# Performance work log

Measured on AMD Instinct MI355X. Metric: run time of the kernel, lower is better.

Reference implementation:

```python
import jax, jax.numpy as jnp
import numpy as np

E, H, KVH, D = 2048, 16, 4, 128      # embed_dim, heads, kv heads, head_dim
HG, R, SYM, VAN = 12, 32, 4, 4       # graph heads, rel_rank, sym heads, vanilla heads
BASE = 10000
EPS = 1e-6


def _rms_norm(x, w):
    # RMSNorm over last dim (head_dim)
    return x * jax.lax.rsqrt(jnp.mean(x * x, axis=-1, keepdims=True) + EPS) * w


def _rotate_half(x):
    x1, x2 = jnp.split(x, 2, axis=-1)
    return jnp.concatenate([-x2, x1], axis=-1)


def _rope(q, k):
    # q, k: [B, H, S, D]
    S = q.shape[2]
    inv_freq = 1.0 / (BASE ** (jnp.arange(0, D, 2, dtype=jnp.float32) / D))
    t = jnp.arange(S, dtype=jnp.float32)
    freqs = jnp.outer(t, inv_freq)                       # [S, D/2]
    emb = jnp.concatenate([freqs, freqs], axis=-1)       # [S, D]
    cos = jnp.cos(emb)[None, None].astype(q.dtype)
    sin = jnp.sin(emb)[None, None].astype(q.dtype)
    return q * cos + _rotate_half(q) * sin, k * cos + _rotate_half(k) * sin


def setup_inputs() -> dict:
    key = jax.random.key(0)
    ks = jax.random.split(key, 9)
    B, S = 1, 2048
    std = 0.02
    return {
        'x': jax.random.normal(ks[0], (B, S, E), jnp.float32),
        'Wq': jax.random.normal(ks[1], (E, E), jnp.float32) * std,
        'Wk': jax.random.normal(ks[2], (KVH * D, E), jnp.float32) * std,
        'Wv': jax.random.normal(ks[3], (KVH * D, E), jnp.float32) * std,
        'Wo': jax.random.normal(ks[4], (E, E), jnp.float32) * std,
        'q_norm_w': jnp.ones((D,), jnp.float32),
        'k_norm_w': jnp.ones((D,), jnp.float32),
        'Wrq': jax.random.normal(ks[5], (HG * R, E), jnp.float32) * 0.01,
        'Wrk': jax.random.normal(ks[6], (HG * R, E), jnp.float32) * 0.01,
        'graph_scale': jax.random.normal(ks[7], (HG,), jnp.float32) * 0.1,
    }


def reference(x, Wq, Wk, Wv, Wo, q_norm_w, k_norm_w, Wrq, Wrk, graph_scale):
    B, S, _ = x.shape
    # projections -> [B, heads, S, D]
    q = (x @ Wq.T).reshape(B, S, H, D).transpose(0, 2, 1, 3)
    k = (x @ Wk.T).reshape(B, S, KVH, D).transpose(0, 2, 1, 3)
    v = (x @ Wv.T).reshape(B, S, KVH, D).transpose(0, 2, 1, 3)
    # QK-norm then RoPE
    q = _rms_norm(q, q_norm_w)
    k = _rms_norm(k, k_norm_w)
    q, k = _rope(q, k)
    # GQA: repeat kv heads
    rep = H // KVH
    k = jnp.repeat(k, rep, axis=1)
    v = jnp.repeat(v, rep, axis=1)
    # low-rank graph bias: [B, HG, S, S]
    Rq = (x @ Wrq.T).reshape(B, S, HG, R).transpose(0, 2, 1, 3)
    Rk = (x @ Wrk.T).reshape(B, S, HG, R).transpose(0, 2, 1, 3)
    bias = jnp.einsum('bhsr,bhtr->bhst', Rq, Rk)
    sym = bias[:, :SYM]
    sym = (sym + sym.transpose(0, 1, 3, 2)) * 0.5
    bias = jnp.concatenate([sym, bias[:, SYM:]], axis=1)
    bias = bias * graph_scale[None, :, None, None]
    # vanilla heads (last VAN heads) get zero bias
    bias = jnp.concatenate([bias, jnp.zeros((B, VAN, S, S), bias.dtype)], axis=1)
    # attention with causal mask
    scale = 1.0 / np.sqrt(D).astype(np.float32)
    scores = jnp.einsum('bhsd,bhtd->bhst', q, k) * scale + bias
    causal = jnp.tril(jnp.ones((S, S), bool))
    scores = jnp.where(causal[None, None], scores, jnp.finfo(scores.dtype).min)
    attn = jax.nn.softmax(scores, axis=-1)
    out = jnp.einsum('bhst,bhtd->bhsd', attn, v)
    out = out.transpose(0, 2, 1, 3).reshape(B, S, E)
    return out @ Wo.T
```

## Files before the change

### kernel.cpp

```cpp
#include <hip/hip_runtime.h>
#include <hip/hip_bf16.h>

typedef __attribute__((ext_vector_type(8))) short short8;
typedef __attribute__((ext_vector_type(4))) float f32x4;
typedef __attribute__((ext_vector_type(4))) unsigned int u32x4;

__device__ __forceinline__ f32x4 mfma16(short8 a, short8 b, f32x4 c) {
  return __builtin_amdgcn_mfma_f32_16x16x32_bf16(a, b, c, 0, 0, 0);
}

__device__ __forceinline__ void gload_lds16(const void* g, void* l) {
  __builtin_amdgcn_global_load_lds(
      (const __attribute__((address_space(1))) void*)g,
      (__attribute__((address_space(3))) void*)l, 16, 0, 0);
}

__device__ __forceinline__ unsigned int bfp(float lo, float hi) {
  return (unsigned int)__builtin_bit_cast(unsigned short, __float2bfloat16(lo)) |
         ((unsigned int)__builtin_bit_cast(unsigned short, __float2bfloat16(hi)) << 16);
}

struct __align__(8) bh4 { __hip_bfloat16 a, b, c, d; };
struct CastSeg { const float* src; __hip_bfloat16* dst; int n4; };
struct CastArgs { CastSeg seg[7]; int tot4; };

__global__ __launch_bounds__(256) void cast_all(CastArgs a) {
  int i = blockIdx.x * 256 + threadIdx.x;
  const int stride = gridDim.x * 256;
  for (; i < a.tot4; i += stride) {
    int j = i, s = 0;
    while (j >= a.seg[s].n4) { j -= a.seg[s].n4; ++s; }
    float4 v = ((const float4*)a.seg[s].src)[j];
    bh4 o{__float2bfloat16(v.x), __float2bfloat16(v.y),
          __float2bfloat16(v.z), __float2bfloat16(v.w)};
    ((bh4*)a.seg[s].dst)[j] = o;
  }
}

__global__ __launch_bounds__(256) void gemm_bt(const __hip_bfloat16* __restrict__ A,
                                               const __hip_bfloat16* __restrict__ B,
                                               float* __restrict__ C,
                                               int N, int K) {
  __shared__ __align__(16) __hip_bfloat16 As[64][32];
  __shared__ __align__(16) __hip_bfloat16 Bs[128][32];

  const int tid = threadIdx.x;
  const int lane = tid & 63, wv = tid >> 6;
  const int wn = wv * 32;
  const int l15 = lane & 15, g = lane >> 4;
  const int mb = blockIdx.y * 64, nb = blockIdx.x * 128;

  const int arow = wv * 16 + (lane >> 2);
  const int brow = wv * 32 + (lane >> 2);
  const int scol = (lane & 3) * 8;
  const __hip_bfloat16* Ap = A + (size_t)(mb + arow) * K + scol;
  const __hip_bfloat16* Bp = B + (size_t)(nb + brow) * K + scol;
  __hip_bfloat16* lA  = &As[wv * 16][0];
  __hip_bfloat16* lB0 = &Bs[wv * 32][0];
  __hip_bfloat16* lB1 = &Bs[wv * 32 + 16][0];

  const f32x4 zf = {0.f, 0.f, 0.f, 0.f};
  f32x4 acc[4][2];
#pragma unroll
  for (int m = 0; m < 4; ++m)
#pragma unroll
    for (int n = 0; n < 2; ++n) acc[m][n] = zf;

  for (int k0 = 0; k0 < K; k0 += 32) {
    __syncthreads();
    gload_lds16(Ap + k0, lA);
    gload_lds16(Bp + k0, lB0);
    gload_lds16(Bp + (size_t)16 * K + k0, lB1);
    __syncthreads();
    short8 af[4], bf[2];
#pragma unroll
    for (int m = 0; m < 4; ++m) af[m] = *(const short8*)&As[m * 16 + l15][g * 8];
#pragma unroll
    for (int n = 0; n < 2; ++n) bf[n] = *(const short8*)&Bs[wn + n * 16 + l15][g * 8];
#pragma unroll
    for (int m = 0; m < 4; ++m)
#pragma unroll
      for (int n = 0; n < 2; ++n) acc[m][n] = mfma16(af[m], bf[n], acc[m][n]);
  }

#pragma unroll
  for (int m = 0; m < 4; ++m)
#pragma unroll
    for (int n = 0; n < 2; ++n)
#pragma unroll
      for (int r = 0; r < 4; ++r)
        C[(size_t)(mb + m * 16 + g * 4 + r) * N + (nb + wn + n * 16 + l15)] =
            acc[m][n][r];
}

__global__ __launch_bounds__(256) void postproc(const float* __restrict__ C1,
                                                const float* __restrict__ qw,
                                                const float* __restrict__ kw,
                                                __hip_bfloat16* __restrict__ qn,
                                                __hip_bfloat16* __restrict__ kn,
                                                __hip_bfloat16* __restrict__ rq,
                                                __hip_bfloat16* __restrict__ rk) {
  constexpr int S = 2048;
  const int s = blockIdx.x;
  const int tid = threadIdx.x;
  const int lane = tid & 63;
  const int wv = tid >> 6;
  const float* row = C1 + (size_t)s * 3840;

  const float f = exp2f(-(float)lane * (13.287712379549449f / 64.0f));
  const float ang = (float)s * f;
  float sn, cs;
  sincosf(ang, &sn, &cs);

  for (int hr = wv; hr < 20; hr += 4) {
    const float* base;
    __hip_bfloat16* dst;
    const float* nw;
    float oscale;
    if (hr < 16) {
      base = row + hr * 128;
      dst = qn + ((size_t)hr * S + s) * 128;
      nw = qw;
      oscale = 0.08838834764831845f;
    } else {
      const int h4 = hr - 16;
      base = row + 2048 + h4 * 128;
      dst = kn + ((size_t)h4 * S + s) * 128;
      nw = kw;
      oscale = 1.0f;
    }
    const float x1 = base[lane], x2 = base[lane + 64];
    float ss = x1 * x1 + x2 * x2;
#pragma unroll
    for (int mk = 1; mk < 64; mk <<= 1) ss += __shfl_xor(ss, mk);
    const float rms = rsqrtf(ss * (1.0f / 128.0f) + 1e-6f);
    const float x1n = x1 * rms * nw[lane];
    const float x2n = x2 * rms * nw[lane + 64];
    dst[lane]      = __float2bfloat16((x1n * cs - x2n * sn) * oscale);
    dst[lane + 64] = __float2bfloat16((x2n * cs + x1n * sn) * oscale);
  }
  for (int i = tid; i < 768; i += 256) {
    if (i < 384) {
      rq[((size_t)(i >> 5) * S + s) * 32 + (i & 31)] = __float2bfloat16(row[3072 + i]);
    } else {
      const int j = i - 384;
      rk[((size_t)(j >> 5) * S + s) * 32 + (j & 31)] = __float2bfloat16(row[3072 + i]);
    }
  }
}

__global__ __launch_bounds__(256) void transpose_v(const float* __restrict__ C1,
                                                   __hip_bfloat16* __restrict__ vt) {
  __shared__ float T[32][129];
  const int b = blockIdx.x;
  const int h4 = b >> 6;
  const int s0 = (b & 63) * 32;
  const int tid = threadIdx.x;
  for (int idx = tid; idx < 4096; idx += 256) {
    const int s = idx >> 7, d = idx & 127;
    T[s][d] = C1[(size_t)(s0 + s) * 3840 + 2560 + h4 * 128 + d];
  }
  __syncthreads();
  for (int j = tid; j < 4096; j += 256) {
    const int d = j >> 5, s = j & 31;
    vt[(size_t)(h4 * 128 + d) * 2048 + s0 + s] = __float2bfloat16(T[s][d]);
  }
}

__global__ __launch_bounds__(256) void attn_kernel(
    const __hip_bfloat16* __restrict__ qn, const __hip_bfloat16* __restrict__ kn,
    const __hip_bfloat16* __restrict__ vt, const __hip_bfloat16* __restrict__ rq,
    const __hip_bfloat16* __restrict__ rk, const float* __restrict__ gsc,
    __hip_bfloat16* __restrict__ ao) {
  constexpr int S = 2048;
  constexpr float L2E = 1.4426950408889634f;
  const int bid = blockIdx.x;
  const int j = bid & 15;
  const int h = ((j & 3) << 2) | (j >> 2);
  const int u = bid >> 4;
  const int qb = (u < 16) ? (31 - u) : (u - 16);
  const int tid = threadIdx.x;
  const int lane = tid & 63;
  const int wv = tid >> 6;
  const int qs = qb * 64 + wv * 16;
  const int l15 = lane & 15, g = lane >> 4;
  const int h4 = h >> 2;
  const bool has_bias = (h < 12);
  const bool symh = (h < 4);
  const float gs = has_bias ? gsc[h] : 0.0f;
  const f32x4 zf = {0.f, 0.f, 0.f, 0.f};

  __shared__ __align__(16) char KsRaw[2][16384];
  __shared__ __align__(16) char VsRaw[2][16384];

  const int sxk = ((tid >> 4) & 7) << 4;
  const int sxv = ((tid >> 3) & 7) << 4;
  const int k_wr = (tid * 16) ^ sxk;
  const int v_wr = (tid * 16) ^ sxv;
  const int kx = (l15 & 7) << 4;

  const __hip_bfloat16* kbase = kn + (size_t)h4 * S * 128;
  const __hip_bfloat16* vbase = vt + (size_t)h4 * 128 * S;
  const __hip_bfloat16* rkp   = rk + (size_t)h * S * 32;
  const __hip_bfloat16* rqp   = rq + (size_t)h * S * 32;

  short8 qf[4];
  {
    const __hip_bfloat16* qrow = qn + ((size_t)h * S + qs + l15) * 128 + g * 8;
#pragma unroll
    for (int kc = 0; kc < 4; ++kc) qf[kc] = *(const short8*)(qrow + kc * 32);
  }
  short8 rqA = {}, rkA = {};
  if (has_bias) rqA = *(const short8*)(rqp + (size_t)(qs + l15) * 32 + g * 8);
  if (symh)     rkA = *(const short8*)(rkp + (size_t)(qs + l15) * 32 + g * 8);

  float lp = 0.0f;
  f32x4 acc[8];
#pragma unroll
  for (int fb = 0; fb < 8; ++fb) acc[fb] = zf;

  const int nt = qb + 1;

  short8 kreg[4], vreg[4];
  auto load_kv = [&](int tb) {
#pragma unroll
    for (int c = 0; c < 4; ++c) {
      kreg[c] = *(const short8*)(kbase + ((size_t)(tb + c * 16 + (tid >> 4))) * 128 + (tid & 15) * 8);
      vreg[c] = *(const short8*)(vbase + ((size_t)(c * 32 + (tid >> 3))) * S + tb + (tid & 7) * 8);
    }
  };

  load_kv(0);
#pragma unroll
  for (int c = 0; c < 4; ++c) {
    *(short8*)(&KsRaw[0][c * 4096 + k_wr]) = kreg[c];
    *(short8*)(&VsRaw[0][c * 4096 + v_wr]) = vreg[c];
  }
  if (nt > 1) load_kv(64);

  short8 rkB[4], rqB[4];
  if (has_bias) {
#pragma unroll
    for (int tf = 0; tf < 4; ++tf)
      rkB[tf] = *(const short8*)(rkp + (size_t)(tf * 16 + l15) * 32 + g * 8);
    if (symh) {
#pragma unroll
      for (int tf = 0; tf < 4; ++tf)
        rqB[tf] = *(const short8*)(rqp + (size_t)(tf * 16 + l15) * 32 + g * 8);
    }
  }

  const int srcA = l15 + ((g & 1) << 5);
  const int srcB = srcA + 16;
  const bool ghi = (g >= 2);

  __syncthreads();

  for (int t = 0; t < nt; ++t) {
    const int tbase = t * 64;
    const int cur = t & 1;
    const char* ksb = &KsRaw[cur][0];
    const char* vsb = &VsRaw[cur][0];

    f32x4 bias4[4];
    if (has_bias) {
#pragma unroll
      for (int tf = 0; tf < 4; ++tf) bias4[tf] = mfma16(rkB[tf], rqA, zf);
      if (symh) {
#pragma unroll
        for (int tf = 0; tf < 4; ++tf) {
          f32x4 b2 = mfma16(rqB[tf], rkA, zf);
#pragma unroll
          for (int r = 0; r < 4; ++r) bias4[tf][r] = 0.5f * (bias4[tf][r] + b2[r]);
        }
      }
      if (t + 1 < nt) {
        const int tb2 = tbase + 64;
#pragma unroll
        for (int tf = 0; tf < 4; ++tf)
          rkB[tf] = *(const short8*)(rkp + (size_t)(tb2 + tf * 16 + l15) * 32 + g * 8);
        if (symh) {
#pragma unroll
          for (int tf = 0; tf < 4; ++tf)
            rqB[tf] = *(const short8*)(rqp + (size_t)(tb2 + tf * 16 + l15) * 32 + g * 8);
        }
      }
    }

    f32x4 sc[4];
#pragma unroll
    for (int tf = 0; tf < 4; ++tf) {
      f32x4 s4 = zf;
#pragma unroll
      for (int kc = 0; kc < 4; ++kc) {
        short8 kf = *(const short8*)(ksb + ((((tf * 16 + l15) << 8) + (kc << 6) + (g << 4)) ^ kx));
        s4 = mfma16(kf, qf[kc], s4);
      }
#pragma unroll
      for (int r = 0; r < 4; ++r) {
        float sv = s4[r];
        if (has_bias) sv += gs * bias4[tf][r];
        if (tbase + tf * 16 + g * 4 + r > qs + l15) sv = -1e30f;
        const float p = exp2f(sv * L2E);
        lp += p;
        sc[tf][r] = p;
      }
    }

    unsigned int pk0[4], pk1[4];
#pragma unroll
    for (int tf = 0; tf < 4; ++tf) {
      pk0[tf] = bfp(sc[tf][0], sc[tf][1]);
      pk1[tf] = bfp(sc[tf][2], sc[tf][3]);
    }
    unsigned int a0[4], a1[4], b0[4], b1[4];
#pragma unroll
    for (int tf = 0; tf < 4; ++tf) {
      a0[tf] = __shfl(pk0[tf], srcA);
      a1[tf] = __shfl(pk1[tf], srcA);
      b0[tf] = __shfl(pk0[tf], srcB);
      b1[tf] = __shfl(pk1[tf], srcB);
    }
    u32x4 w0 = {ghi ? a0[1] : a0[0], ghi ? a1[1] : a1[0],
                ghi ? b0[1] : b0[0], ghi ? b1[1] : b1[0]};
    u32x4 w1 = {ghi ? a0[3] : a0[2], ghi ? a1[3] : a1[2],
                ghi ? b0[3] : b0[2], ghi ? b1[3] : b1[2]};
    const short8 pa0 = __builtin_bit_cast(short8, w0);
    const short8 pa1 = __builtin_bit_cast(short8, w1);

#pragma unroll
    for (int fb = 0; fb < 8; ++fb) {
      short8 v0 = *(const short8*)(vsb + ((((fb * 16 + l15) << 7) + (g << 4)) ^ kx));
      short8 v1 = *(const short8*)(vsb + ((((fb * 16 + l15) << 7) + 64 + (g << 4)) ^ kx));
      acc[fb] = mfma16(pa0, v0, acc[fb]);
      acc[fb] = mfma16(pa1, v1, acc[fb]);
    }

    if (t + 1 < nt) {
      char* ksw = &KsRaw[cur ^ 1][0];
      char* vsw = &VsRaw[cur ^ 1][0];
#pragma unroll
      for (int c = 0; c < 4; ++c) {
        *(short8*)(ksw + c * 4096 + k_wr) = kreg[c];
        *(short8*)(vsw + c * 4096 + v_wr) = vreg[c];
      }
      if (t + 2 < nt) load_kv(tbase + 128);
    }
    __syncthreads();
  }

  float lt = lp;
  lt += __shfl_xor(lt, 16);
  lt += __shfl_xor(lt, 32);
  const float linv = 1.0f / lt;
  float lr[4];
#pragma unroll
  for (int r = 0; r < 4; ++r) lr[r] = __shfl(linv, g * 4 + r);

#pragma unroll
  for (int fb = 0; fb < 8; ++fb)
#pragma unroll
    for (int r = 0; r < 4; ++r) {
      const int srow = qs + g * 4 + r;
      ao[(size_t)srow * 2048 + h * 128 + fb * 16 + l15] =
          __float2bfloat16(acc[fb][r] * lr[r]);
    }
}

extern "C" void kernel_launch(void* const* d_in, const int* in_sizes, int n_in,
                              void* d_out, int out_size, void* d_ws, size_t ws_size,
                              hipStream_t stream) {
  (void)in_sizes; (void)n_in; (void)out_size; (void)ws_size;
  constexpr int S = 2048, E = 2048;

  const float* x   = (const float*)d_in[0];
  const float* Wq  = (const float*)d_in[1];
  const float* Wk  = (const float*)d_in[2];
  const float* Wv  = (const float*)d_in[3];
  const float* Wo  = (const float*)d_in[4];
  const float* qw  = (const float*)d_in[5];
  const float* kw  = (const float*)d_in[6];
  const float* Wrq = (const float*)d_in[7];
  const float* Wrk = (const float*)d_in[8];
  const float* gsc = (const float*)d_in[9];
  float* out = (float*)d_out;

  char* ws = (char*)d_ws;
  size_t off = 0;
  auto alloc = [&](size_t bytes) -> void* {
    void* p = ws + off;
    off += (bytes + 255) & ~(size_t)255;
    return p;
  };
  __hip_bfloat16* xb   = (__hip_bfloat16*)alloc((size_t)S * E * 2);
  __hip_bfloat16* Wall = (__hip_bfloat16*)alloc((size_t)3840 * E * 2);
  __hip_bfloat16* Wob  = (__hip_bfloat16*)alloc((size_t)E * E * 2);
  __hip_bfloat16* qnb  = (__hip_bfloat16*)alloc((size_t)16 * S * 128 * 2);
  __hip_bfloat16* knb  = (__hip_bfloat16*)alloc((size_t)4 * S * 128 * 2);
  __hip_bfloat16* vtb  = (__hip_bfloat16*)alloc((size_t)4 * 128 * S * 2);
  __hip_bfloat16* rqb  = (__hip_bfloat16*)alloc((size_t)12 * S * 32 * 2);
  __hip_bfloat16* rkb  = (__hip_bfloat16*)alloc((size_t)12 * S * 32 * 2);
  float* C1            = (float*)alloc((size_t)S * 3840 * 4);
  __hip_bfloat16* ao   = (__hip_bfloat16*)C1;

  CastArgs ca;
  ca.seg[0] = {x,   xb,                      (int)((size_t)S * E / 4)};
  ca.seg[1] = {Wq,  Wall,                    (int)((size_t)E * E / 4)};
  ca.seg[2] = {Wk,  Wall + (size_t)2048 * E, (int)((size_t)512 * E / 4)};
  ca.seg[3] = {Wv,  Wall + (size_t)2560 * E, (int)((size_t)512 * E / 4)};
  ca.seg[4] = {Wrq, Wall + (size_t)3072 * E, (int)((size_t)384 * E / 4)};
  ca.seg[5] = {Wrk, Wall + (size_t)3456 * E, (int)((size_t)384 * E / 4)};
  ca.seg[6] = {Wo,  Wob,                     (int)((size_t)E * E / 4)};
  ca.tot4 = 0;
  for (int i = 0; i < 7; ++i) ca.tot4 += ca.seg[i].n4;
  cast_all<<<dim3(2048), dim3(256), 0, stream>>>(ca);

  gemm_bt<<<dim3(30, 32), dim3(256), 0, stream>>>(xb, Wall, C1, 3840, E);
  postproc<<<dim3(2048), dim3(256), 0, stream>>>(C1, qw, kw, qnb, knb, rqb, rkb);
  transpose_v<<<dim3(256), dim3(256), 0, stream>>>(C1, vtb);
  attn_kernel<<<dim3(512), dim3(256), 0, stream>>>(qnb, knb, vtb, rqb, rkb, gsc, ao);
  gemm_bt<<<dim3(16, 32), dim3(256), 0, stream>>>(ao, Wob, out, E, E);
}
```

Baseline: 293.1 us.

## Split attention KV loop across two wave groups and merge partial outputs

The attention block grows to 512 threads, and two groups of four waves each process alternating KV tiles (split-K within the block). Each group keeps its own LDS buffers, and at the end group 1 writes its partial accumulators and row sums to LDS so group 0 can combine them. The causal mask is now evaluated only on diagonal tiles. This doubles the waves in flight per query tile to raise CU utilization on the long causal rows, at the cost of more LDS, two barriers per step, an extra reduction, and the loss of the previous double-buffered overlap within a group.

Measured after the change: 506.5 us. 72.8% more time.

```diff
diff --git a/kernel.cpp b/kernel.cpp
--- a/kernel.cpp
+++ b/kernel.cpp
@@ -167,7 +167,7 @@
   }
 }
 
-__global__ __launch_bounds__(256) void attn_kernel(
+__global__ __launch_bounds__(512, 4) void attn_kernel(
     const __hip_bfloat16* __restrict__ qn, const __hip_bfloat16* __restrict__ kn,
     const __hip_bfloat16* __restrict__ vt, const __hip_bfloat16* __restrict__ rq,
     const __hip_bfloat16* __restrict__ rk, const float* __restrict__ gsc,
@@ -182,7 +182,10 @@
   const int tid = threadIdx.x;
   const int lane = tid & 63;
   const int wv = tid >> 6;
-  const int qs = qb * 64 + wv * 16;
+  const int w4 = wv & 3;
+  const int gp = wv >> 2;
+  const int gtid = tid & 255;
+  const int qs = qb * 64 + w4 * 16;
   const int l15 = lane & 15, g = lane >> 4;
   const int h4 = h >> 2;
   const bool has_bias = (h < 12);
@@ -190,13 +193,14 @@
   const float gs = has_bias ? gsc[h] : 0.0f;
   const f32x4 zf = {0.f, 0.f, 0.f, 0.f};
 
-  __shared__ __align__(16) char KsRaw[2][16384];
-  __shared__ __align__(16) char VsRaw[2][16384];
-
-  const int sxk = ((tid >> 4) & 7) << 4;
-  const int sxv = ((tid >> 3) & 7) << 4;
-  const int k_wr = (tid * 16) ^ sxk;
-  const int v_wr = (tid * 16) ^ sxv;
+  __shared__ __align__(16) char smem[65536];
+  char* ksBuf = smem + gp * 32768;
+  char* vsBuf = smem + gp * 32768 + 16384;
+
+  const int sxk = ((gtid >> 4) & 7) << 4;
+  const int sxv = ((gtid >> 3) & 7) << 4;
+  const int k_wr = (gtid * 16) ^ sxk;
+  const int v_wr = (gtid * 16) ^ sxv;
   const int kx = (l15 & 7) << 4;
 
   const __hip_bfloat16* kbase = kn + (size_t)h4 * S * 128;
@@ -220,33 +224,27 @@
   for (int fb = 0; fb < 8; ++fb) acc[fb] = zf;
 
   const int nt = qb + 1;
+  const int nsteps = (nt + 1) >> 1;
 
   short8 kreg[4], vreg[4];
   auto load_kv = [&](int tb) {
 #pragma unroll
     for (int c = 0; c < 4; ++c) {
-      kreg[c] = *(const short8*)(kbase + ((size_t)(tb + c * 16 + (tid >> 4))) * 128 + (tid & 15) * 8);
-      vreg[c] = *(const short8*)(vbase + ((size_t)(c * 32 + (tid >> 3))) * S + tb + (tid & 7) * 8);
+      kreg[c] = *(const short8*)(kbase + ((size_t)(tb + c * 16 + (gtid >> 4))) * 128 + (gtid & 15) * 8);
+      vreg[c] = *(const short8*)(vbase + ((size_t)(c * 32 + (gtid >> 3))) * S + tb + (gtid & 7) * 8);
     }
   };
 
-  load_kv(0);
-#pragma unroll
-  for (int c = 0; c < 4; ++c) {
-    *(short8*)(&KsRaw[0][c * 4096 + k_wr]) = kreg[c];
-    *(short8*)(&VsRaw[0][c * 4096 + v_wr]) = vreg[c];
-  }
-  if (nt > 1) load_kv(64);
-
+  if (gp < nt) load_kv(gp * 64);
   short8 rkB[4], rqB[4];
   if (has_bias) {
 #pragma unroll
     for (int tf = 0; tf < 4; ++tf)
-      rkB[tf] = *(const short8*)(rkp + (size_t)(tf * 16 + l15) * 32 + g * 8);
+      rkB[tf] = *(const short8*)(rkp + (size_t)(gp * 64 + tf * 16 + l15) * 32 + g * 8);
     if (symh) {
 #pragma unroll
       for (int tf = 0; tf < 4; ++tf)
-        rqB[tf] = *(const short8*)(rqp + (size_t)(tf * 16 + l15) * 32 + g * 8);
+        rqB[tf] = *(const short8*)(rqp + (size_t)(gp * 64 + tf * 16 + l15) * 32 + g * 8);
     }
   }
 
@@ -254,13 +252,23 @@
   const int srcB = srcA + 16;
   const bool ghi = (g >= 2);
 
-  __syncthreads();
-
-  for (int t = 0; t < nt; ++t) {
+  for (int step = 0; step < nsteps; ++step) {
+    const int t = 2 * step + gp;
+    const bool active = (t < nt);
     const int tbase = t * 64;
-    const int cur = t & 1;
-    const char* ksb = &KsRaw[cur][0];
-    const char* vsb = &VsRaw[cur][0];
+
+    __syncthreads();
+    if (active) {
+#pragma unroll
+      for (int c = 0; c < 4; ++c) {
+        *(short8*)(ksBuf + c * 4096 + k_wr) = kreg[c];
+        *(short8*)(vsBuf + c * 4096 + v_wr) = vreg[c];
+      }
+      if (t + 2 < nt) load_kv(tbase + 128);
+    }
+    __syncthreads();
+
+    if (!active) continue;
 
     f32x4 bias4[4];
     if (has_bias) {
@@ -274,8 +282,8 @@
           for (int r = 0; r < 4; ++r) bias4[tf][r] = 0.5f * (bias4[tf][r] + b2[r]);
         }
       }
-      if (t + 1 < nt) {
-        const int tb2 = tbase + 64;
+      if (t + 2 < nt) {
+        const int tb2 = tbase + 128;
 #pragma unroll
         for (int tf = 0; tf < 4; ++tf)
           rkB[tf] = *(const short8*)(rkp + (size_t)(tb2 + tf * 16 + l15) * 32 + g * 8);
@@ -288,22 +296,34 @@
     }
 
     f32x4 sc[4];
+    const bool needmask = (tbase + 63 > qs);
 #pragma unroll
     for (int tf = 0; tf < 4; ++tf) {
       f32x4 s4 = zf;
 #pragma unroll
       for (int kc = 0; kc < 4; ++kc) {
-        short8 kf = *(const short8*)(ksb + ((((tf * 16 + l15) << 8) + (kc << 6) + (g << 4)) ^ kx));
+        short8 kf = *(const short8*)(ksBuf + ((((tf * 16 + l15) << 8) + (kc << 6) + (g << 4)) ^ kx));
         s4 = mfma16(kf, qf[kc], s4);
       }
-#pragma unroll
-      for (int r = 0; r < 4; ++r) {
-        float sv = s4[r];
-        if (has_bias) sv += gs * bias4[tf][r];
-        if (tbase + tf * 16 + g * 4 + r > qs + l15) sv = -1e30f;
-        const float p = exp2f(sv * L2E);
-        lp += p;
-        sc[tf][r] = p;
+      if (needmask) {
+#pragma unroll
+        for (int r = 0; r < 4; ++r) {
+          float sv = s4[r];
+          if (has_bias) sv += gs * bias4[tf][r];
+          if (tbase + tf * 16 + g * 4 + r > qs + l15) sv = -1e30f;
+          const float p = exp2f(sv * L2E);
+          lp += p;
+          sc[tf][r] = p;
+        }
+      } else {
+#pragma unroll
+        for (int r = 0; r < 4; ++r) {
+          float sv = s4[r];
+          if (has_bias) sv += gs * bias4[tf][r];
+          const float p = exp2f(sv * L2E);
+          lp += p;
+          sc[tf][r] = p;
+        }
       }
     }
 
@@ -330,41 +350,45 @@
 
 #pragma unroll
     for (int fb = 0; fb < 8; ++fb) {
-      short8 v0 = *(const short8*)(vsb + ((((fb * 16 + l15) << 7) + (g << 4)) ^ kx));
-      short8 v1 = *(const short8*)(vsb + ((((fb * 16 + l15) << 7) + 64 + (g << 4)) ^ kx));
+      short8 v0 = *(const short8*)(vsBuf + ((((fb * 16 + l15) << 7) + (g << 4)) ^ kx));
+      short8 v1 = *(const short8*)(vsBuf + ((((fb * 16 + l15) << 7) + 64 + (g << 4)) ^ kx));
       acc[fb] = mfma16(pa0, v0, acc[fb]);
       acc[fb] = mfma16(pa1, v1, acc[fb]);
     }
-
-    if (t + 1 < nt) {
-      char* ksw = &KsRaw[cur ^ 1][0];
-      char* vsw = &VsRaw[cur ^ 1][0];
-#pragma unroll
-      for (int c = 0; c < 4; ++c) {
-        *(short8*)(ksw + c * 4096 + k_wr) = kreg[c];
-        *(short8*)(vsw + c * 4096 + v_wr) = vreg[c];
-      }
-      if (t + 2 < nt) load_kv(tbase + 128);
-    }
-    __syncthreads();
-  }
-
-  float lt = lp;
-  lt += __shfl_xor(lt, 16);
-  lt += __shfl_xor(lt, 32);
-  const float linv = 1.0f / lt;
-  float lr[4];
-#pragma unroll
-  for (int r = 0; r < 4; ++r) lr[r] = __shfl(linv, g * 4 + r);
-
-#pragma unroll
-  for (int fb = 0; fb < 8; ++fb)
-#pragma unroll
-    for (int r = 0; r < 4; ++r) {
-      const int srow = qs + g * 4 + r;
-      ao[(size_t)srow * 2048 + h * 128 + fb * 16 + l15] =
-          __float2bfloat16(acc[fb][r] * lr[r]);
-    }
+  }
+
+  float ltg = lp;
+  ltg += __shfl_xor(ltg, 16);
+  ltg += __shfl_xor(ltg, 32);
+
+  __syncthreads();
+  float* Oc = (float*)smem;
+  float* Lg = (float*)(smem + 64 * 132 * 4);
+  if (gp == 1) {
+#pragma unroll
+    for (int fb = 0; fb < 8; ++fb)
+#pragma unroll
+      for (int r = 0; r < 4; ++r)
+        Oc[(size_t)(w4 * 16 + g * 4 + r) * 132 + fb * 16 + l15] = acc[fb][r];
+    if (lane < 16) Lg[w4 * 16 + l15] = ltg;
+  }
+  __syncthreads();
+  if (gp == 0) {
+    const float lt = ltg + Lg[w4 * 16 + l15];
+    const float linv = 1.0f / lt;
+    float lr[4];
+#pragma unroll
+    for (int r = 0; r < 4; ++r) lr[r] = __shfl(linv, g * 4 + r);
+#pragma unroll
+    for (int fb = 0; fb < 8; ++fb)
+#pragma unroll
+      for (int r = 0; r < 4; ++r) {
+        const float o = acc[fb][r] + Oc[(size_t)(w4 * 16 + g * 4 + r) * 132 + fb * 16 + l15];
+        const int srow = qs + g * 4 + r;
+        ao[(size_t)srow * 2048 + h * 128 + fb * 16 + l15] =
+            __float2bfloat16(o * lr[r]);
+      }
+  }
 }
 
 extern "C" void kernel_launch(void* const* d_in, const int* in_sizes, int n_in,
@@ -418,6 +442,6 @@
   gemm_bt<<<dim3(30, 32), dim3(256), 0, stream>>>(xb, Wall, C1, 3840, E);
   postproc<<<dim3(2048), dim3(256), 0, stream>>>(C1, qw, kw, qnb, knb, rqb, rkb);
   transpose_v<<<dim3(256), dim3(256), 0, stream>>>(C1, vtb);
-  attn_kernel<<<dim3(512), dim3(256), 0, stream>>>(qnb, knb, vtb, rqb, rkb, gsc, ao);
+  attn_kernel<<<dim3(512), dim3(512), 0, stream>>>(qnb, knb, vtb, rqb, rkb, gsc, ao);
   gemm_bt<<<dim3(16, 32), dim3(256), 0, stream>>>(ao, Wob, out, E, E);
 }
```
